# Kernel optimization log

Hardware: AMD Instinct MI355X
Metric: run time of the kernel (lower is better)

The kernel has to match this reference:

```python
import jax, jax.numpy as jnp
import numpy as np

IN_F = 4096
OUT_F = 8192
BLOCK = 16   # block_dim
KEEP = 8     # keep_k low-frequency modes kept per block
NLEV = 256   # n_levels


def dct_inv_basis(keep_k, n):
    # Orthonormal DCT-II synthesis basis, rows = kept frequencies k, cols = time index t.
    k = jnp.arange(keep_k, dtype=jnp.float32)[:, None]
    t = jnp.arange(n, dtype=jnp.float32)[None, :]
    B = jnp.cos(jnp.pi * (t + 0.5) * k / n) * jnp.sqrt(2.0 / n)
    scale = jnp.where(jnp.arange(keep_k) == 0, 1.0 / jnp.sqrt(2.0), 1.0)
    return B * scale[:, None]  # [keep_k, block_dim]


def setup_inputs() -> dict:
    key = jax.random.key(0)
    k1, k2, k3, k4, k5 = jax.random.split(key, 5)
    n_blocks = OUT_F * IN_F // BLOCK  # 2097152
    x = jax.random.normal(k1, (32, 8, IN_F), jnp.float32)
    idx = jax.random.randint(k2, (n_blocks, KEEP), 0, NLEV, jnp.int32)
    c_min = jax.random.normal(k3, (KEEP,), jnp.float32)
    c_range = jax.random.uniform(k4, (KEEP,), jnp.float32) + 0.1
    bias = jax.random.normal(k5, (OUT_F,), jnp.float32)
    return {"x": x, "idx": idx, "c_min": c_min, "c_range": c_range, "bias": bias}


def reference(x, idx, c_min, c_range, bias):
    # Affine dequant of kept frequency codes: [n_blocks, keep_k]
    coeffs = idx.astype(jnp.float32) / (NLEV - 1) * c_range + c_min
    # Inverse DCT per block (high-frequency modes are implicitly zero)
    B = dct_inv_basis(KEEP, BLOCK)              # [keep_k, block_dim]
    W = (coeffs @ B).reshape(OUT_F, IN_F)       # dense dequantized weight
    return x @ W.T + bias
```

## Files before the change

### kernel.cpp

```cpp
#include <hip/hip_runtime.h>


typedef __attribute__((ext_vector_type(8))) short bf16x8;
typedef __attribute__((ext_vector_type(4))) float f32x4;

#define K_TOT   2048
#define N_TOT   8192
#define NT      32
#define NCHUNK  8
#define SPC     8
#define LDS_CH  16384

__device__ __forceinline__ unsigned short f2bf_rn(float f) {
    unsigned u = __float_as_uint(f);
    u += 0x7FFFu + ((u >> 16) & 1u);
    return (unsigned short)(u >> 16);
}
__device__ __forceinline__ unsigned pack2(int a, int b) {
    unsigned ua = __float_as_uint((float)a);
    unsigned ub = __float_as_uint((float)b);
    return __builtin_amdgcn_perm(ub, ua, 0x07060302u);
}

__device__ __forceinline__ void lds_barrier() {
    asm volatile("" ::: "memory");
    __builtin_amdgcn_s_waitcnt(0xC07F);
    __builtin_amdgcn_s_barrier();
    asm volatile("" ::: "memory");
}

__global__ __launch_bounds__(256) void prep_kernel(
    const float* __restrict__ x, const float* __restrict__ c_min,
    const float* __restrict__ c_range, unsigned short* __restrict__ Y2f,
    float* __restrict__ corr)
{
    __shared__ float Bk[8][16];
    __shared__ float scmin[8];
    __shared__ float ss[8];
    __shared__ float red[4];
    const int tid = threadIdx.x;
    const int m = blockIdx.x;
    if (tid < 128) {
        int k = tid >> 4, t = tid & 15;
        float v = cosf(3.14159265358979f * (t + 0.5f) * (float)k / 16.0f)
                  * 0.353553390593274f;
        if (k == 0) v *= 0.707106781186548f;
        Bk[k][t] = v;
    }
    if (tid < 8) {
        scmin[tid] = c_min[tid];
        ss[tid] = c_range[tid] * (1.0f / 255.0f);
    }
    __syncthreads();

    const float* xp = x + (long)m * 4096 + tid * 16;
    float xs[16];
#pragma unroll
    for (int q = 0; q < 4; ++q) {
        float4 v = *(const float4*)(xp + q * 4);
        xs[q * 4 + 0] = v.x; xs[q * 4 + 1] = v.y;
        xs[q * 4 + 2] = v.z; xs[q * 4 + 3] = v.w;
    }
    float partial = 0.0f;
    unsigned short yo[8];
#pragma unroll
    for (int k = 0; k < 8; ++k) {
        float y = 0.0f;
#pragma unroll
        for (int t = 0; t < 16; ++t) y += xs[t] * Bk[k][t];
        partial += y * scmin[k];
        yo[k] = f2bf_rn(y * ss[k]);
    }
    uint4 pk;
    pk.x = (unsigned)yo[0] | ((unsigned)yo[1] << 16);
    pk.y = (unsigned)yo[2] | ((unsigned)yo[3] << 16);
    pk.z = (unsigned)yo[4] | ((unsigned)yo[5] << 16);
    pk.w = (unsigned)yo[6] | ((unsigned)yo[7] << 16);
    {
        const int mg = m >> 4, fr = m & 15, kc = tid >> 2, fq = tid & 3;
        unsigned short* dst = Y2f + ((long)((mg * 64 + kc) * 64) + fq * 16 + fr) * 8;
        *(uint4*)dst = pk;
    }
#pragma unroll
    for (int off = 32; off > 0; off >>= 1)
        partial += __shfl_down(partial, off, 64);
    if ((tid & 63) == 0) red[tid >> 6] = partial;
    __syncthreads();
    if (tid == 0) corr[m] = red[0] + red[1] + red[2] + red[3];
}

struct Stage { int4 v[4]; };

__global__ __launch_bounds__(512, 2) void gemm_kernel(
    const unsigned short* __restrict__ Y2f, const int* __restrict__ idx,
    const float* __restrict__ bias, const float* __restrict__ corr,
    float* __restrict__ out)
{
    __shared__ char lds[2 * LDS_CH];

    const int tid  = threadIdx.x;
    const int wave = tid >> 6;
    const int lane = tid & 63;
    const int fr   = lane & 15;
    const int fq   = lane >> 4;
    const int o0   = blockIdx.x * NT;

    const int* sBase = idx + (long)(o0 + wave) * K_TOT + lane * 4;
    const int dstBase = (((lane >> 3) * 4 + ((lane & 7) >> 1)) * 32 + wave) * 16
                        + (lane & 1) * 8;

    const bf16x8* aB[2];
    aB[0] = (const bf16x8*)Y2f + (long)((wave * 2 + 0) * 64) * 64 + lane;
    aB[1] = (const bf16x8*)Y2f + (long)((wave * 2 + 1) * 64) * 64 + lane;

    f32x4 acc[2][2] = {{{0.f,0.f,0.f,0.f},{0.f,0.f,0.f,0.f}},
                       {{0.f,0.f,0.f,0.f},{0.f,0.f,0.f,0.f}}};

    Stage S[2];

#define STAGE_LOAD(slot, ch)                                              \
    {                                                                     \
        _Pragma("unroll")                                                 \
        for (int l = 0; l < 4; ++l)                                       \
            S[slot].v[l] = *(const int4*)(sBase + l * 8 * K_TOT + (ch) * 256); \
    }

#define STAGE_WRITE(slot, ch)                                             \
    {                                                                     \
        char* buf = lds + ((ch) & 1) * LDS_CH;                            \
        _Pragma("unroll")                                                 \
        for (int l = 0; l < 4; ++l) {                                     \
            uint2 w;                                                      \
            w.x = pack2(S[slot].v[l].x, S[slot].v[l].y);                  \
            w.y = pack2(S[slot].v[l].z, S[slot].v[l].w);                  \
            *(uint2*)(buf + dstBase + l * 128) = w;                       \
        }                                                                 \
    }

#define COMPUTE(ch)                                                       \
    {                                                                     \
        const char* buf = lds + ((ch) & 1) * LDS_CH;                      \
        bf16x8 a[SPC][2];                                                 \
        _Pragma("unroll")                                                 \
        for (int s = 0; s < SPC; ++s) {                                   \
            a[s][0] = aB[0][((ch) * SPC + s) * 64];                       \
            a[s][1] = aB[1][((ch) * SPC + s) * 64];                       \
        }                                                                 \
        bf16x8 b[2][2];                                                   \
        _Pragma("unroll")                                                 \
        for (int g = 0; g < 2; ++g)                                       \
            b[0][g] = *(const bf16x8*)(buf + ((0 * 4 + fq) * 32 + g * 16 + fr) * 16); \
        _Pragma("unroll")                                                 \
        for (int s = 0; s < SPC; ++s) {                                   \
            if (s + 1 < SPC) {                                            \
                _Pragma("unroll")                                         \
                for (int g = 0; g < 2; ++g)                               \
                    b[(s + 1) & 1][g] = *(const bf16x8*)(buf +            \
                        (((s + 1) * 4 + fq) * 32 + g * 16 + fr) * 16);    \
            }                                                             \
            _Pragma("unroll")                                             \
            for (int mt = 0; mt < 2; ++mt) {                              \
                _Pragma("unroll")                                         \
                for (int g = 0; g < 2; ++g)                               \
                    acc[mt][g] = __builtin_amdgcn_mfma_f32_16x16x32_bf16( \
                        a[s][mt], b[s & 1][g], acc[mt][g], 0, 0, 0);      \
            }                                                             \
        }                                                                 \
    }

    STAGE_LOAD(0, 0)
    STAGE_LOAD(1, 1)
    STAGE_WRITE(0, 0)
    lds_barrier();

#pragma unroll
    for (int c = 0; c < NCHUNK - 2; ++c) {
        COMPUTE(c)
        STAGE_LOAD(c & 1, c + 2)
        STAGE_WRITE((c + 1) & 1, c + 1)
        lds_barrier();
    }
    COMPUTE(NCHUNK - 2)
    STAGE_WRITE((NCHUNK - 1) & 1, NCHUNK - 1)
    lds_barrier();
    COMPUTE(NCHUNK - 1)

#pragma unroll
    for (int mt = 0; mt < 2; ++mt) {
#pragma unroll
        for (int g = 0; g < 2; ++g) {
            const int col = o0 + g * 16 + fr;
            const float bv = bias[col];
#pragma unroll
            for (int r = 0; r < 4; ++r) {
                const int row = (wave * 2 + mt) * 16 + fq * 4 + r;
                out[(long)row * N_TOT + col] = acc[mt][g][r] + bv + corr[row];
            }
        }
    }
#undef STAGE_LOAD
#undef STAGE_WRITE
#undef COMPUTE
}

extern "C" void kernel_launch(void* const* d_in, const int* in_sizes, int n_in,
                              void* d_out, int out_size, void* d_ws, size_t ws_size,
                              hipStream_t stream) {
    const float* x       = (const float*)d_in[0];
    const int*   idx     = (const int*)d_in[1];
    const float* c_min   = (const float*)d_in[2];
    const float* c_range = (const float*)d_in[3];
    const float* bias    = (const float*)d_in[4];
    float* out = (float*)d_out;

    unsigned short* Y2f = (unsigned short*)d_ws;
    float* corr = (float*)((char*)d_ws + (size_t)256 * K_TOT * 2);

    prep_kernel<<<256, 256, 0, stream>>>(x, c_min, c_range, Y2f, corr);
    gemm_kernel<<<N_TOT / NT, 512, 0, stream>>>(Y2f, idx, bias, corr, out);
}
```

Measured before the change: 125.8 us.

## Split GEMM M dimension across two 256-thread blocks with XOR-swizzled LDS

The GEMM now launches 512 blocks of 256 threads instead of 256 blocks of 512. Each block covers half of the 256 rows, so both halves of a column tile decode the same idx codes into LDS. The LDS layout for the decoded weights changes to row-major with an XOR swizzle, meant to cut bank conflicts on the fragment reads. The staging becomes a single 8-register buffer, loaded after the LDS write. In exchange, every idx element is read from global memory twice and each wave does twice as many staging loads.

```diff
diff --git a/kernel.cpp b/kernel.cpp
--- a/kernel.cpp
+++ b/kernel.cpp
@@ -89,9 +89,7 @@
     if (tid == 0) corr[m] = red[0] + red[1] + red[2] + red[3];
 }
 
-struct Stage { int4 v[4]; };
-
-__global__ __launch_bounds__(512, 2) void gemm_kernel(
+__global__ __launch_bounds__(256, 2) void gemm_kernel(
     const unsigned short* __restrict__ Y2f, const int* __restrict__ idx,
     const float* __restrict__ bias, const float* __restrict__ corr,
     float* __restrict__ out)
@@ -103,39 +101,44 @@
     const int lane = tid & 63;
     const int fr   = lane & 15;
     const int fq   = lane >> 4;
-    const int o0   = blockIdx.x * NT;
+    const int o0   = (blockIdx.x & 255) * NT;
+    const int h    = blockIdx.x >> 8;
 
     const int* sBase = idx + (long)(o0 + wave) * K_TOT + lane * 4;
-    const int dstBase = (((lane >> 3) * 4 + ((lane & 7) >> 1)) * 32 + wave) * 16
-                        + (lane & 1) * 8;
-
-    const bf16x8* aB[2];
-    aB[0] = (const bf16x8*)Y2f + (long)((wave * 2 + 0) * 64) * 64 + lane;
-    aB[1] = (const bf16x8*)Y2f + (long)((wave * 2 + 1) * 64) * 64 + lane;
+    const int wslot = lane >> 1;
+    const int wj    = (lane & 1) * 8;
+
+    const bf16x8* aF[2];
+    aF[0] = (const bf16x8*)Y2f + (long)((h * 8 + wave * 2 + 0) * 64) * 64 + lane;
+    aF[1] = (const bf16x8*)Y2f + (long)((h * 8 + wave * 2 + 1) * 64) * 64 + lane;
 
     f32x4 acc[2][2] = {{{0.f,0.f,0.f,0.f},{0.f,0.f,0.f,0.f}},
                        {{0.f,0.f,0.f,0.f},{0.f,0.f,0.f,0.f}}};
-
-    Stage S[2];
-
-#define STAGE_LOAD(slot, ch)                                              \
+    int4 S[8];
+
+#define STAGE_LOAD(ch)                                                    \
     {                                                                     \
         _Pragma("unroll")                                                 \
-        for (int l = 0; l < 4; ++l)                                       \
-            S[slot].v[l] = *(const int4*)(sBase + l * 8 * K_TOT + (ch) * 256); \
-    }
-
-#define STAGE_WRITE(slot, ch)                                             \
+        for (int l = 0; l < 8; ++l)                                       \
+            S[l] = *(const int4*)(sBase + (long)l * 4 * K_TOT + (ch) * 256); \
+    }
+
+#define STAGE_WRITE(ch)                                                   \
     {                                                                     \
         char* buf = lds + ((ch) & 1) * LDS_CH;                            \
         _Pragma("unroll")                                                 \
-        for (int l = 0; l < 4; ++l) {                                     \
+        for (int l = 0; l < 8; ++l) {                                     \
+            const int c = wave + l * 4;                                   \
             uint2 w;                                                      \
-            w.x = pack2(S[slot].v[l].x, S[slot].v[l].y);                  \
-            w.y = pack2(S[slot].v[l].z, S[slot].v[l].w);                  \
-            *(uint2*)(buf + dstBase + l * 128) = w;                       \
+            w.x = pack2(S[l].x, S[l].y);                                  \
+            w.y = pack2(S[l].z, S[l].w);                                  \
+            *(uint2*)(buf + c * 512 + ((wslot ^ c) * 16) + wj) = w;       \
         }                                                                 \
     }
+
+#define BREAD(buf, s, g)                                                  \
+    (*(const bf16x8*)((buf) + (g * 16 + fr) * 512 +                       \
+                      ((((s) * 4 + fq) ^ (g * 16 + fr)) * 16)))
 
 #define COMPUTE(ch)                                                       \
     {                                                                     \
@@ -143,45 +146,41 @@
         bf16x8 a[SPC][2];                                                 \
         _Pragma("unroll")                                                 \
         for (int s = 0; s < SPC; ++s) {                                   \
-            a[s][0] = aB[0][((ch) * SPC + s) * 64];                       \
-            a[s][1] = aB[1][((ch) * SPC + s) * 64];                       \
+            a[s][0] = aF[0][((ch) * SPC + s) * 64];                       \
+            a[s][1] = aF[1][((ch) * SPC + s) * 64];                       \
         }                                                                 \
         bf16x8 b[2][2];                                                   \
-        _Pragma("unroll")                                                 \
-        for (int g = 0; g < 2; ++g)                                       \
-            b[0][g] = *(const bf16x8*)(buf + ((0 * 4 + fq) * 32 + g * 16 + fr) * 16); \
+        b[0][0] = BREAD(buf, 0, 0);                                       \
+        b[0][1] = BREAD(buf, 0, 1);                                       \
         _Pragma("unroll")                                                 \
         for (int s = 0; s < SPC; ++s) {                                   \
             if (s + 1 < SPC) {                                            \
-                _Pragma("unroll")                                         \
-                for (int g = 0; g < 2; ++g)                               \
-                    b[(s + 1) & 1][g] = *(const bf16x8*)(buf +            \
-                        (((s + 1) * 4 + fq) * 32 + g * 16 + fr) * 16);    \
+                b[(s + 1) & 1][0] = BREAD(buf, (s + 1), 0);               \
+                b[(s + 1) & 1][1] = BREAD(buf, (s + 1), 1);               \
             }                                                             \
             _Pragma("unroll")                                             \
-            for (int mt = 0; mt < 2; ++mt) {                              \
+            for (int mt = 0; mt < 2; ++mt)                                \
                 _Pragma("unroll")                                         \
                 for (int g = 0; g < 2; ++g)                               \
                     acc[mt][g] = __builtin_amdgcn_mfma_f32_16x16x32_bf16( \
                         a[s][mt], b[s & 1][g], acc[mt][g], 0, 0, 0);      \
-            }                                                             \
         }                                                                 \
     }
 
-    STAGE_LOAD(0, 0)
-    STAGE_LOAD(1, 1)
-    STAGE_WRITE(0, 0)
+    STAGE_LOAD(0)
+    STAGE_WRITE(0)
+    STAGE_LOAD(1)
     lds_barrier();
 
 #pragma unroll
     for (int c = 0; c < NCHUNK - 2; ++c) {
         COMPUTE(c)
-        STAGE_LOAD(c & 1, c + 2)
-        STAGE_WRITE((c + 1) & 1, c + 1)
+        STAGE_WRITE(c + 1)
+        STAGE_LOAD(c + 2)
         lds_barrier();
     }
     COMPUTE(NCHUNK - 2)
-    STAGE_WRITE((NCHUNK - 1) & 1, NCHUNK - 1)
+    STAGE_WRITE(NCHUNK - 1)
     lds_barrier();
     COMPUTE(NCHUNK - 1)
 
@@ -191,15 +190,16 @@
         for (int g = 0; g < 2; ++g) {
             const int col = o0 + g * 16 + fr;
             const float bv = bias[col];
-#pragma unroll
-            for (int r = 0; r < 4; ++r) {
-                const int row = (wave * 2 + mt) * 16 + fq * 4 + r;
-                out[(long)row * N_TOT + col] = acc[mt][g][r] + bv + corr[row];
-            }
+            const int row0 = (h * 8 + wave * 2 + mt) * 16 + fq * 4;
+#pragma unroll
+            for (int r = 0; r < 4; ++r)
+                out[(long)(row0 + r) * N_TOT + col] =
+                    acc[mt][g][r] + bv + corr[row0 + r];
         }
     }
 #undef STAGE_LOAD
 #undef STAGE_WRITE
+#undef BREAD
 #undef COMPUTE
 }
 
@@ -217,5 +217,5 @@
     float* corr = (float*)((char*)d_ws + (size_t)256 * K_TOT * 2);
 
     prep_kernel<<<256, 256, 0, stream>>>(x, c_min, c_range, Y2f, corr);
-    gemm_kernel<<<N_TOT / NT, 512, 0, stream>>>(Y2f, idx, bias, corr, out);
-}
+    gemm_kernel<<<512, 256, 0, stream>>>(Y2f, idx, bias, corr, out);
+}
```

After: 124.5 us. About the same (-1.0%).
